# Performance work log

Hardware: AMD Instinct MI355X
Metric: run time of the kernel (lower is better)

## Reference

```python
import jax, jax.numpy as jnp
import numpy as np

NUM_HEADS = 16
ROPE_BASE = 10000.0


def _rope_cos_sin(seq_len, head_dim, dtype):
    inv_freq = 1.0 / (ROPE_BASE ** (jnp.arange(0, head_dim, 2, dtype=jnp.float32) / head_dim))
    freqs = jnp.arange(seq_len, dtype=jnp.float32)[:, None] * inv_freq[None, :]  # [L, hd/2]
    return jnp.cos(freqs).astype(dtype), jnp.sin(freqs).astype(dtype)


def _apply_rope(t, cos, sin):
    # t: [B, H, L, hd]; cos/sin: [L, hd/2] broadcast over B,H
    x1 = t[..., ::2]
    x2 = t[..., 1::2]
    r1 = x1 * cos - x2 * sin
    r2 = x1 * sin + x2 * cos
    return jnp.stack([r1, r2], axis=-1).reshape(t.shape)


def setup_inputs() -> dict:
    key = jax.random.key(0)
    k1, k2, k3 = jax.random.split(key, 3)
    B, L, D = 2, 2048, 1024
    x = jax.random.normal(k1, (B, L, D), dtype=jnp.float32)
    W_qkv = jax.random.normal(k2, (3 * D, D), dtype=jnp.float32) * (D ** -0.5)
    W_out = jax.random.normal(k3, (D, D), dtype=jnp.float32) * (D ** -0.5)
    return {"x": x, "W_qkv": W_qkv, "W_out": W_out}


def reference(x, W_qkv, W_out):
    B, L, D = x.shape
    H = NUM_HEADS
    hd = D // H
    scale = hd ** -0.5

    qkv = x @ W_qkv.T                              # [B, L, 3D]
    qkv = qkv.reshape(B, L, 3, H, hd)
    qkv = jnp.transpose(qkv, (2, 0, 3, 1, 4))      # [3, B, H, L, hd]
    q, k, v = qkv[0], qkv[1], qkv[2]

    cos, sin = _rope_cos_sin(L, hd, x.dtype)
    q = _apply_rope(q, cos, sin)
    k = _apply_rope(k, cos, sin)

    logits = jnp.einsum("bhqd,bhkd->bhqk", q, k) * scale
    attn = jax.nn.softmax(logits, axis=-1)         # dropout p=0.0 -> identity
    out = jnp.einsum("bhqk,bhkd->bhqd", attn, v)   # [B, H, L, hd]
    out = jnp.transpose(out, (0, 2, 1, 3)).reshape(B, L, D)
    return out @ W_out.T
```

## Files before the change

### kernel.cpp

```cpp
#include <hip/hip_runtime.h>
#include <hip/hip_bf16.h>
#include <stdint.h>


typedef __bf16 bf16x8 __attribute__((ext_vector_type(8)));
typedef float f32x4 __attribute__((ext_vector_type(4)));

__device__ __forceinline__ unsigned short f2bf(float f) {
  union { float f; unsigned int u; } v; v.f = f;
  unsigned int r = v.u + 0x7FFFu + ((v.u >> 16) & 1u);
  return (unsigned short)(r >> 16);
}
__device__ __forceinline__ float b2f(unsigned short u) {
  union { unsigned int u; float f; } v; v.u = ((unsigned int)u) << 16;
  return v.f;
}

__device__ __forceinline__ void gl2lds16(const void* gptr, void* lptr) {
  __builtin_amdgcn_global_load_lds(
      (const __attribute__((address_space(1))) unsigned int*)gptr,
      (__attribute__((address_space(3))) unsigned int*)lptr, 16, 0, 0);
}

__global__ void cvt_all(const float4* __restrict__ x,
                        const float4* __restrict__ wq,
                        const float4* __restrict__ wo,
                        ushort4* __restrict__ xb,
                        ushort4* __restrict__ wqb,
                        ushort4* __restrict__ wob) {
  int i = blockIdx.x * 256 + threadIdx.x;
  float4 v; ushort4* dst; int j;
  if (i < 1048576)      { v = x[i];            dst = xb;  j = i; }
  else if (i < 1835008) { v = wq[i - 1048576]; dst = wqb; j = i - 1048576; }
  else                  { v = wo[i - 1835008]; dst = wob; j = i - 1835008; }
  ushort4 o;
  o.x = f2bf(v.x); o.y = f2bf(v.y); o.z = f2bf(v.z); o.w = f2bf(v.w);
  dst[j] = o;
}

__global__ __launch_bounds__(256) void gemm_bt(
    const __hip_bfloat16* __restrict__ A,
    const __hip_bfloat16* __restrict__ B,
    unsigned short* __restrict__ C, int M, int N, int K) {
  __shared__ __align__(16) char lds[32768];
  const int tid = threadIdx.x;
  const int lane = tid & 63;
  const int wave = tid >> 6;
  const int wm = (wave >> 1) * 64, wn = (wave & 1) * 64;
  const int g = lane >> 4, lr = lane & 15;
  const int m0 = blockIdx.y * 128, n0 = blockIdx.x * 128;
  f32x4 acc[4][4] = {};

  const size_t ldb = (size_t)K * 2;
  const int c0 = tid, c1 = tid + 256;
  const int r0 = c0 >> 2, cb0 = (c0 & 3) * 16;
  const int r1 = c1 >> 2, cb1 = (c1 & 3) * 16;
  const char* A0 = (const char*)(A + (size_t)m0 * K) + (size_t)r0 * ldb + cb0;
  const char* A1 = (const char*)(A + (size_t)m0 * K) + (size_t)r1 * ldb + cb1;
  const char* B0 = (const char*)(B + (size_t)n0 * K) + (size_t)r0 * ldb + cb0;
  const char* B1 = (const char*)(B + (size_t)n0 * K) + (size_t)r1 * ldb + cb1;

  auto stage = [&](int bo) {
    gl2lds16(A0, lds + bo + c0 * 16);
    gl2lds16(A1, lds + bo + c1 * 16);
    gl2lds16(B0, lds + bo + 8192 + c0 * 16);
    gl2lds16(B1, lds + bo + 8192 + c1 * 16);
    A0 += 64; A1 += 64; B0 += 64; B1 += 64;
  };

  stage(0);

  const int NSTEP = K / 32;
  for (int kt = 0; kt < NSTEP; ++kt) {
    const int bo = (kt & 1) * 16384;
    if (kt + 1 < NSTEP) {
      stage(bo ^ 16384);
      asm volatile("s_waitcnt vmcnt(4)" ::: "memory");
    } else {
      asm volatile("s_waitcnt vmcnt(0)" ::: "memory");
    }
    __builtin_amdgcn_s_barrier();

    bf16x8 af[4], bfr[4];
#pragma unroll
    for (int i = 0; i < 4; ++i)
      af[i] = *(const bf16x8*)(lds + bo + (wm + i * 16 + lr) * 64 + g * 16);
#pragma unroll
    for (int i = 0; i < 4; ++i)
      bfr[i] = *(const bf16x8*)(lds + bo + 8192 + (wn + i * 16 + lr) * 64 + g * 16);
    __builtin_amdgcn_s_setprio(1);
#pragma unroll
    for (int i = 0; i < 4; ++i)
#pragma unroll
      for (int j = 0; j < 4; ++j)
        acc[i][j] = __builtin_amdgcn_mfma_f32_16x16x32_bf16(af[i], bfr[j], acc[i][j], 0, 0, 0);
    __builtin_amdgcn_s_setprio(0);
    asm volatile("s_waitcnt lgkmcnt(0)" ::: "memory");
    __builtin_amdgcn_s_barrier();
  }

#pragma unroll
  for (int i = 0; i < 4; ++i) {
#pragma unroll
    for (int j = 0; j < 4; ++j) {
      int n = n0 + wn + j * 16 + lr;
#pragma unroll
      for (int r = 0; r < 4; ++r) {
        int m = m0 + wm + i * 16 + g * 4 + r;
        C[(size_t)m * N + n] = f2bf(acc[i][j][r]);
      }
    }
  }
}

__global__ __launch_bounds__(256) void gemm2_64(
    const __hip_bfloat16* __restrict__ A,
    const __hip_bfloat16* __restrict__ B,
    float* __restrict__ C, int M, int N, int K) {
  __shared__ __align__(16) char lds[16384];
  const int tid = threadIdx.x, lane = tid & 63, w = tid >> 6;
  const int g = lane >> 4, lr = lane & 15;
  const int n0 = blockIdx.x * 64, m0 = blockIdx.y * 64;
  f32x4 acc[4] = {};

  const size_t ld = (size_t)K * 2;
  const int o16 = tid * 16;
  const int s = o16 ^ (((o16 >> 6) & 3) << 4);
  const int srow = s >> 6, scolb = s & 63;
  const char* Asrc = (const char*)(A + (size_t)m0 * K) + (size_t)srow * ld + scolb;
  const char* Bsrc = (const char*)(B + (size_t)n0 * K) + (size_t)srow * ld + scolb;

  auto stage = [&](int bo) {
    gl2lds16(Asrc, lds + bo + o16);
    gl2lds16(Bsrc, lds + 8192 + bo + o16);
    Asrc += 64; Bsrc += 64;
  };

  stage(0);

  const int swz = (lr & 3) << 4;
  const int NSTEP = K / 32;
  for (int kt = 0; kt < NSTEP; ++kt) {
    const int bo = (kt & 1) * 4096;
    if (kt + 1 < NSTEP) {
      stage(bo ^ 4096);
      asm volatile("s_waitcnt vmcnt(2)" ::: "memory");
    } else {
      asm volatile("s_waitcnt vmcnt(0)" ::: "memory");
    }
    __builtin_amdgcn_s_barrier();

    bf16x8 af = *(const bf16x8*)(lds + bo + (((w * 16 + lr) * 64 + g * 16) ^ swz));
    __builtin_amdgcn_s_setprio(1);
#pragma unroll
    for (int j = 0; j < 4; ++j) {
      bf16x8 bf = *(const bf16x8*)(lds + 8192 + bo + (((j * 16 + lr) * 64 + g * 16) ^ swz));
      acc[j] = __builtin_amdgcn_mfma_f32_16x16x32_bf16(af, bf, acc[j], 0, 0, 0);
    }
    __builtin_amdgcn_s_setprio(0);
    asm volatile("s_waitcnt lgkmcnt(0)" ::: "memory");
    __builtin_amdgcn_s_barrier();
  }

#pragma unroll
  for (int j = 0; j < 4; ++j) {
    int n = n0 + j * 16 + lr;
#pragma unroll
    for (int r = 0; r < 4; ++r) {
      int m = m0 + w * 16 + g * 4 + r;
      C[(size_t)m * N + n] = acc[j][r];
    }
  }
}

__global__ void rope_scatter(const __hip_bfloat16* __restrict__ qkv,
                             __hip_bfloat16* __restrict__ Qs,
                             __hip_bfloat16* __restrict__ Ks,
                             __hip_bfloat16* __restrict__ Vt) {
  const int t = blockIdx.x * 256 + threadIdx.x;
  const int i = t & 31;
  const int lc = (t >> 5) & 255;
  const int h = (t >> 13) & 15;
  const int b = t >> 17;
  const float inv_freq = powf(10000.0f, -(float)i * (1.0f / 32.0f));
  const float QSCALE = 0.125f * 1.44269504088896f;
  const unsigned short* qk = (const unsigned short*)qkv;
  unsigned short v0[8], v1[8];
#pragma unroll
  for (int j = 0; j < 8; ++j) {
    const int l = lc * 8 + j;
    const size_t row = ((size_t)(b * 2048 + l)) * 3072;
    float s, c;
    sincosf((float)l * inv_freq, &s, &c);
    ushort2 qp = *(const ushort2*)(qk + row + h * 64 + 2 * i);
    ushort2 kp = *(const ushort2*)(qk + row + 1024 + h * 64 + 2 * i);
    ushort2 vp = *(const ushort2*)(qk + row + 2048 + h * 64 + 2 * i);
    float x1 = b2f(qp.x), x2 = b2f(qp.y);
    float y1 = b2f(kp.x), y2 = b2f(kp.y);
    size_t oidx = (((size_t)(b * 16 + h)) * 2048 + l) * 64 + 2 * i;
    ushort2 qo, ko;
    qo.x = f2bf((x1 * c - x2 * s) * QSCALE);
    qo.y = f2bf((x1 * s + x2 * c) * QSCALE);
    ko.x = f2bf(y1 * c - y2 * s);
    ko.y = f2bf(y1 * s + y2 * c);
    *(ushort2*)((unsigned short*)Qs + oidx) = qo;
    *(ushort2*)((unsigned short*)Ks + oidx) = ko;
    v0[j] = vp.x; v1[j] = vp.y;
  }
  const int m = lc & 3;
  const int colA = ((m & 1) << 4) + ((m >> 1) << 2);
  unsigned short* Vtu = (unsigned short*)Vt;
  const size_t vrow0 = (((size_t)(b * 16 + h)) * 64 + 2 * i) * 2048 + (lc >> 2) * 32;
  const size_t vrow1 = vrow0 + 2048;
  *(ushort4*)(Vtu + vrow0 + colA)     = make_ushort4(v0[0], v0[1], v0[2], v0[3]);
  *(ushort4*)(Vtu + vrow0 + colA + 8) = make_ushort4(v0[4], v0[5], v0[6], v0[7]);
  *(ushort4*)(Vtu + vrow1 + colA)     = make_ushort4(v1[0], v1[1], v1[2], v1[3]);
  *(ushort4*)(Vtu + vrow1 + colA + 8) = make_ushort4(v1[4], v1[5], v1[6], v1[7]);
}

__global__ __launch_bounds__(256, 4) void attn_fwd(
    const __hip_bfloat16* __restrict__ Qs,
    const __hip_bfloat16* __restrict__ Ks,
    const __hip_bfloat16* __restrict__ Vt,
    float* __restrict__ Opart,
    float2* __restrict__ Ml) {
  constexpr int L = 2048;
  __shared__ __align__(16) char lds[32768];
  const int tid = threadIdx.x, lane = tid & 63, w = tid >> 6;
  const int g = lane >> 4, lr = lane & 15;
  const int blk = blockIdx.x;
  const int xcd = blk & 7, slot = blk >> 3;
  const int bh = xcd * 4 + (slot >> 5);
  const int rem = slot & 31;
  const int qt = rem >> 1, half = rem & 1;
  const int q0 = qt * 128 + w * 32 + lr;
  const int kt0 = half * 16;

  const __hip_bfloat16* Qr = Qs + ((size_t)bh * L + q0) * 64;
  bf16x8 qf[2][2];
  qf[0][0] = *(const bf16x8*)(Qr + g * 8);
  qf[0][1] = *(const bf16x8*)(Qr + 32 + g * 8);
  qf[1][0] = *(const bf16x8*)(Qr + 16 * 64 + g * 8);
  qf[1][1] = *(const bf16x8*)(Qr + 16 * 64 + 32 + g * 8);

  bf16x8 onesf;
#pragma unroll
  for (int j = 0; j < 8; ++j) onesf[j] = (__bf16)1.0f;

  const int xmask = (lr & 7) << 4;
  const int loff0 = ((g * 16) ^ (xmask & 0x30)) + (xmask & 0x40);
  const int kb0 = lr * 128 + loff0;
  const int kb1 = kb0 ^ 64;

  const int c0 = tid * 16, c1 = c0 + 4096;
  const int os0 = c0 ^ (((c0 >> 7) & 7) << 4);
  const int os1 = c1 ^ (((c1 >> 7) & 7) << 4);
  const char* Kb = (const char*)(Ks + (size_t)bh * L * 64) + (size_t)kt0 * 8192;
  const char* Vb = (const char*)(Vt + (size_t)bh * 64 * L) + kt0 * 128;
  const char* KsrcA = Kb + os0;
  const char* KsrcB = Kb + os1;
  const char* VsrcA = Vb + (size_t)(os0 >> 7) * (L * 2) + (os0 & 127);
  const char* VsrcB = Vb + (size_t)(os1 >> 7) * (L * 2) + (os1 & 127);

  auto stage = [&](int bo) {
    gl2lds16(KsrcA, lds + bo + c0);
    gl2lds16(KsrcB, lds + bo + c1);
    gl2lds16(VsrcA, lds + 16384 + bo + c0);
    gl2lds16(VsrcB, lds + 16384 + bo + c1);
    KsrcA += 8192; KsrcB += 8192; VsrcA += 128; VsrcB += 128;
  };

  f32x4 oacc[2][4] = {};
  f32x4 lacc[2] = {};
  float mrun[2] = {-1e30f, -1e30f};

  stage(0);

  for (int kt = 0; kt < 16; ++kt) {
    const int bo = (kt & 1) * 8192;
    if (kt + 1 < 16) {
      stage(bo ^ 8192);
      asm volatile("s_waitcnt vmcnt(4)" ::: "memory");
    } else {
      asm volatile("s_waitcnt vmcnt(0)" ::: "memory");
    }
    __builtin_amdgcn_s_barrier();

    const char* Kc = lds + bo;
    const char* Vc = lds + 16384 + bo;

    f32x4 sacc[2][4] = {};
    __builtin_amdgcn_s_setprio(1);
#pragma unroll
    for (int mf = 0; mf < 4; ++mf) {
      bf16x8 a0 = *(const bf16x8*)(Kc + kb0 + mf * 2048);
      bf16x8 a1 = *(const bf16x8*)(Kc + kb1 + mf * 2048);
      sacc[0][mf] = __builtin_amdgcn_mfma_f32_16x16x32_bf16(a0, qf[0][0], sacc[0][mf], 0, 0, 0);
      sacc[0][mf] = __builtin_amdgcn_mfma_f32_16x16x32_bf16(a1, qf[0][1], sacc[0][mf], 0, 0, 0);
      sacc[1][mf] = __builtin_amdgcn_mfma_f32_16x16x32_bf16(a0, qf[1][0], sacc[1][mf], 0, 0, 0);
      sacc[1][mf] = __builtin_amdgcn_mfma_f32_16x16x32_bf16(a1, qf[1][1], sacc[1][mf], 0, 0, 0);
    }
    __builtin_amdgcn_s_setprio(0);

#pragma unroll
    for (int qg = 0; qg < 2; ++qg) {
      float a0 = fmaxf(fmaxf(sacc[qg][0][0], sacc[qg][0][1]), sacc[qg][0][2]);
      float a1 = fmaxf(fmaxf(sacc[qg][0][3], sacc[qg][1][0]), sacc[qg][1][1]);
      float a2 = fmaxf(fmaxf(sacc[qg][1][2], sacc[qg][1][3]), sacc[qg][2][0]);
      float a3 = fmaxf(fmaxf(sacc[qg][2][1], sacc[qg][2][2]), sacc[qg][2][3]);
      float a4 = fmaxf(fmaxf(sacc[qg][3][0], sacc[qg][3][1]), sacc[qg][3][2]);
      float b0 = fmaxf(fmaxf(a0, a1), a2);
      float b1 = fmaxf(fmaxf(a3, a4), sacc[qg][3][3]);
      float lmax = fmaxf(b0, b1);
      if (__any(lmax > mrun[qg] + 8.0f)) {
        float tmax = fmaxf(lmax, __shfl_xor(lmax, 16));
        tmax = fmaxf(tmax, __shfl_xor(tmax, 32));
        float mnew = fmaxf(mrun[qg], tmax);
        float al = __builtin_amdgcn_exp2f(mrun[qg] - mnew);
        mrun[qg] = mnew;
        lacc[qg] *= al;
#pragma unroll
        for (int d = 0; d < 4; ++d) oacc[qg][d] = oacc[qg][d] * al;
      }
#pragma unroll
      for (int mf = 0; mf < 4; ++mf) {
        sacc[qg][mf][0] = __builtin_amdgcn_exp2f(sacc[qg][mf][0] - mrun[qg]);
        sacc[qg][mf][1] = __builtin_amdgcn_exp2f(sacc[qg][mf][1] - mrun[qg]);
        sacc[qg][mf][2] = __builtin_amdgcn_exp2f(sacc[qg][mf][2] - mrun[qg]);
        sacc[qg][mf][3] = __builtin_amdgcn_exp2f(sacc[qg][mf][3] - mrun[qg]);
      }
    }

#pragma unroll
    for (int ks = 0; ks < 2; ++ks) {
      bf16x8 pf[2];
#pragma unroll
      for (int qg = 0; qg < 2; ++qg) {
#pragma unroll
        for (int j = 0; j < 4; ++j) {
          pf[qg][j]     = (__bf16)sacc[qg][2 * ks][j];
          pf[qg][4 + j] = (__bf16)sacc[qg][2 * ks + 1][j];
        }
      }
      const int kb = ks ? kb1 : kb0;
      __builtin_amdgcn_s_setprio(1);
      lacc[0] = __builtin_amdgcn_mfma_f32_16x16x32_bf16(onesf, pf[0], lacc[0], 0, 0, 0);
      lacc[1] = __builtin_amdgcn_mfma_f32_16x16x32_bf16(onesf, pf[1], lacc[1], 0, 0, 0);
#pragma unroll
      for (int df = 0; df < 4; ++df) {
        bf16x8 a = *(const bf16x8*)(Vc + kb + df * 2048);
        oacc[0][df] = __builtin_amdgcn_mfma_f32_16x16x32_bf16(a, pf[0], oacc[0][df], 0, 0, 0);
        oacc[1][df] = __builtin_amdgcn_mfma_f32_16x16x32_bf16(a, pf[1], oacc[1][df], 0, 0, 0);
      }
      __builtin_amdgcn_s_setprio(0);
    }
    asm volatile("s_waitcnt lgkmcnt(0)" ::: "memory");
    __builtin_amdgcn_s_barrier();
  }

#pragma unroll
  for (int qg = 0; qg < 2; ++qg) {
    const size_t rowi = ((size_t)bh * L + q0 + qg * 16) * 2 + half;
    float* Od = Opart + rowi * 64;
#pragma unroll
    for (int df = 0; df < 4; ++df)
      *(f32x4*)(Od + df * 16 + g * 4) = oacc[qg][df];
    if (g == 0) {
      float2 ml; ml.x = mrun[qg]; ml.y = lacc[qg][0];
      Ml[rowi] = ml;
    }
  }
}

__global__ __launch_bounds__(256) void attn_reduce(
    const float* __restrict__ Opart, const float2* __restrict__ Ml,
    unsigned short* __restrict__ Ob) {
  int t = blockIdx.x * 256 + threadIdx.x;
  int d = t & 63;
  int r = t >> 6;
  float2 a = Ml[2 * r], b = Ml[2 * r + 1];
  float m = fmaxf(a.x, b.x);
  float w0 = __builtin_amdgcn_exp2f(a.x - m);
  float w1 = __builtin_amdgcn_exp2f(b.x - m);
  float l = a.y * w0 + b.y * w1;
  float o = Opart[(size_t)(2 * r) * 64 + d] * w0 + Opart[(size_t)(2 * r + 1) * 64 + d] * w1;
  float out = o / l;
  int bh = r >> 11, qq = r & 2047;
  Ob[(((size_t)(bh >> 4) * 2048 + qq)) * 1024 + (bh & 15) * 64 + d] = f2bf(out);
}

extern "C" void kernel_launch(void* const* d_in, const int* in_sizes, int n_in,
                              void* d_out, int out_size, void* d_ws, size_t ws_size,
                              hipStream_t stream) {
  (void)in_sizes; (void)n_in; (void)out_size; (void)ws_size;
  const float* x    = (const float*)d_in[0];
  const float* wqkv = (const float*)d_in[1];
  const float* wout = (const float*)d_in[2];

  char* ws = (char*)d_ws;
  auto* wob   = (__hip_bfloat16*)(ws + ((size_t)0u  << 20));
  auto* Qsb   = (__hip_bfloat16*)(ws + ((size_t)2u  << 20));
  auto* Ob    = (__hip_bfloat16*)(ws + ((size_t)2u  << 20));
  auto* Ksb   = (__hip_bfloat16*)(ws + ((size_t)10u << 20));
  auto* Vtb   = (__hip_bfloat16*)(ws + ((size_t)18u << 20));
  auto* qkvb  = (__hip_bfloat16*)(ws + ((size_t)26u << 20));
  auto* Opart = (float*)         (ws + ((size_t)26u << 20));
  auto* xb    = (__hip_bfloat16*)(ws + ((size_t)50u << 20));
  auto* wqb   = (__hip_bfloat16*)(ws + ((size_t)58u << 20));
  auto* Mlp   = (float2*)        (ws + ((size_t)58u << 20));

  cvt_all<<<8192, 256, 0, stream>>>((const float4*)x, (const float4*)wqkv,
                                    (const float4*)wout,
                                    (ushort4*)xb, (ushort4*)wqb, (ushort4*)wob);
  gemm_bt<<<dim3(24, 32), 256, 0, stream>>>(xb, wqb, (unsigned short*)qkvb,
                                            4096, 3072, 1024);
  rope_scatter<<<1024, 256, 0, stream>>>(qkvb, Qsb, Ksb, Vtb);
  attn_fwd<<<1024, 256, 0, stream>>>(Qsb, Ksb, Vtb, Opart, Mlp);
  attn_reduce<<<16384, 256, 0, stream>>>(Opart, Mlp, (unsigned short*)Ob);
  gemm2_64<<<dim3(16, 64), 256, 0, stream>>>(Ob, wob, (float*)d_out,
                                             4096, 1024, 1024);
}
```

Before: 133.5 us.

## Fuse RoPE, Q/K scatter and V transpose into QKV GEMM epilogue

Result: no change. 131.0 us (-1.8%).

```diff
diff --git a/kernel.cpp b/kernel.cpp
--- a/kernel.cpp
+++ b/kernel.cpp
@@ -27,8 +27,18 @@
                         const float4* __restrict__ wo,
                         ushort4* __restrict__ xb,
                         ushort4* __restrict__ wqb,
-                        ushort4* __restrict__ wob) {
+                        ushort4* __restrict__ wob,
+                        float2* __restrict__ tab) {
   int i = blockIdx.x * 256 + threadIdx.x;
+  if (i >= 2097152) {
+    int t = i - 2097152;
+    int l = t >> 5, fi = t & 31;
+    float inv_freq = powf(10000.0f, -(float)fi / 32.0f);
+    float s, c;
+    sincosf((float)l * inv_freq, &s, &c);
+    tab[t] = make_float2(c, s);
+    return;
+  }
   float4 v; ushort4* dst; int j;
   if (i < 1048576)      { v = x[i];            dst = xb;  j = i; }
   else if (i < 1835008) { v = wq[i - 1048576]; dst = wqb; j = i - 1048576; }
@@ -38,10 +48,13 @@
   dst[j] = o;
 }
 
-__global__ __launch_bounds__(256) void gemm_bt(
+__global__ __launch_bounds__(256) void gemm1_fused(
     const __hip_bfloat16* __restrict__ A,
     const __hip_bfloat16* __restrict__ B,
-    unsigned short* __restrict__ C, int M, int N, int K) {
+    unsigned short* __restrict__ Qs,
+    unsigned short* __restrict__ Ks,
+    unsigned short* __restrict__ Vt,
+    const float2* __restrict__ tab, int K) {
   __shared__ __align__(16) char lds[32768];
   const int tid = threadIdx.x;
   const int lane = tid & 63;
@@ -99,15 +112,44 @@
     __builtin_amdgcn_s_barrier();
   }
 
-#pragma unroll
-  for (int i = 0; i < 4; ++i) {
+  const int sel = n0 >> 10;
+  if (sel <= 1) {
+    const float qscale = (sel == 0) ? 0.125f * 1.44269504088896f : 1.0f;
+    unsigned short* dst = (sel == 0) ? Qs : Ks;
 #pragma unroll
     for (int j = 0; j < 4; ++j) {
-      int n = n0 + wn + j * 16 + lr;
-#pragma unroll
-      for (int r = 0; r < 4; ++r) {
-        int m = m0 + wm + i * 16 + g * 4 + r;
-        C[(size_t)m * N + n] = f2bf(acc[i][j][r]);
+      const int nn = (n0 + wn + j * 16 + lr) & 1023;
+      const int h = nn >> 6, d = nn & 63;
+      const float2* tabrow = tab + (d >> 1);
+      const float sgn = (d & 1) ? 1.0f : -1.0f;
+#pragma unroll
+      for (int i = 0; i < 4; ++i) {
+#pragma unroll
+        for (int r = 0; r < 4; ++r) {
+          const int m = m0 + wm + i * 16 + g * 4 + r;
+          const int l = m & 2047, b = m >> 11;
+          float own = acc[i][j][r];
+          float part = __shfl_xor(own, 1);
+          float2 cs = tabrow[l * 32];
+          float out = fmaf(cs.x, own, sgn * cs.y * part) * qscale;
+          dst[((size_t)((b * 16 + h) * 2048 + l)) * 64 + d] = f2bf(out);
+        }
+      }
+    }
+  } else {
+#pragma unroll
+    for (int j = 0; j < 4; ++j) {
+      const int nn = (n0 + wn + j * 16 + lr) & 1023;
+      const int h = nn >> 6, d = nn & 63;
+#pragma unroll
+      for (int i = 0; i < 4; ++i) {
+        const int mb = m0 + wm + i * 16 + g * 4;
+        const int l0 = mb & 2047, b = mb >> 11;
+        const int pl = (l0 & ~31) + 8 * ((l0 & 15) >> 2) + 4 * ((l0 >> 4) & 1) + (l0 & 3);
+        ushort4 v4;
+        v4.x = f2bf(acc[i][j][0]); v4.y = f2bf(acc[i][j][1]);
+        v4.z = f2bf(acc[i][j][2]); v4.w = f2bf(acc[i][j][3]);
+        *(ushort4*)(Vt + ((size_t)((b * 16 + h) * 64 + d)) * 2048 + pl) = v4;
       }
     }
   }
@@ -171,51 +213,6 @@
       C[(size_t)m * N + n] = acc[j][r];
     }
   }
-}
-
-__global__ void rope_scatter(const __hip_bfloat16* __restrict__ qkv,
-                             __hip_bfloat16* __restrict__ Qs,
-                             __hip_bfloat16* __restrict__ Ks,
-                             __hip_bfloat16* __restrict__ Vt) {
-  const int t = blockIdx.x * 256 + threadIdx.x;
-  const int i = t & 31;
-  const int lc = (t >> 5) & 255;
-  const int h = (t >> 13) & 15;
-  const int b = t >> 17;
-  const float inv_freq = powf(10000.0f, -(float)i * (1.0f / 32.0f));
-  const float QSCALE = 0.125f * 1.44269504088896f;
-  const unsigned short* qk = (const unsigned short*)qkv;
-  unsigned short v0[8], v1[8];
-#pragma unroll
-  for (int j = 0; j < 8; ++j) {
-    const int l = lc * 8 + j;
-    const size_t row = ((size_t)(b * 2048 + l)) * 3072;
-    float s, c;
-    sincosf((float)l * inv_freq, &s, &c);
-    ushort2 qp = *(const ushort2*)(qk + row + h * 64 + 2 * i);
-    ushort2 kp = *(const ushort2*)(qk + row + 1024 + h * 64 + 2 * i);
-    ushort2 vp = *(const ushort2*)(qk + row + 2048 + h * 64 + 2 * i);
-    float x1 = b2f(qp.x), x2 = b2f(qp.y);
-    float y1 = b2f(kp.x), y2 = b2f(kp.y);
-    size_t oidx = (((size_t)(b * 16 + h)) * 2048 + l) * 64 + 2 * i;
-    ushort2 qo, ko;
-    qo.x = f2bf((x1 * c - x2 * s) * QSCALE);
-    qo.y = f2bf((x1 * s + x2 * c) * QSCALE);
-    ko.x = f2bf(y1 * c - y2 * s);
-    ko.y = f2bf(y1 * s + y2 * c);
-    *(ushort2*)((unsigned short*)Qs + oidx) = qo;
-    *(ushort2*)((unsigned short*)Ks + oidx) = ko;
-    v0[j] = vp.x; v1[j] = vp.y;
-  }
-  const int m = lc & 3;
-  const int colA = ((m & 1) << 4) + ((m >> 1) << 2);
-  unsigned short* Vtu = (unsigned short*)Vt;
-  const size_t vrow0 = (((size_t)(b * 16 + h)) * 64 + 2 * i) * 2048 + (lc >> 2) * 32;
-  const size_t vrow1 = vrow0 + 2048;
-  *(ushort4*)(Vtu + vrow0 + colA)     = make_ushort4(v0[0], v0[1], v0[2], v0[3]);
-  *(ushort4*)(Vtu + vrow0 + colA + 8) = make_ushort4(v0[4], v0[5], v0[6], v0[7]);
-  *(ushort4*)(Vtu + vrow1 + colA)     = make_ushort4(v1[0], v1[1], v1[2], v1[3]);
-  *(ushort4*)(Vtu + vrow1 + colA + 8) = make_ushort4(v1[4], v1[5], v1[6], v1[7]);
 }
 
 __global__ __launch_bounds__(256, 4) void attn_fwd(
@@ -403,18 +400,21 @@
   auto* Ob    = (__hip_bfloat16*)(ws + ((size_t)2u  << 20));
   auto* Ksb   = (__hip_bfloat16*)(ws + ((size_t)10u << 20));
   auto* Vtb   = (__hip_bfloat16*)(ws + ((size_t)18u << 20));
-  auto* qkvb  = (__hip_bfloat16*)(ws + ((size_t)26u << 20));
   auto* Opart = (float*)         (ws + ((size_t)26u << 20));
   auto* xb    = (__hip_bfloat16*)(ws + ((size_t)50u << 20));
-  auto* wqb   = (__hip_bfloat16*)(ws + ((size_t)58u << 20));
   auto* Mlp   = (float2*)        (ws + ((size_t)58u << 20));
-
-  cvt_all<<<8192, 256, 0, stream>>>((const float4*)x, (const float4*)wqkv,
+  auto* tab   = (float2*)        (ws + ((size_t)59u << 20));
+  auto* wqb   = (__hip_bfloat16*)(ws + (((size_t)59u << 20) + ((size_t)1u << 19)));
+
+  cvt_all<<<8448, 256, 0, stream>>>((const float4*)x, (const float4*)wqkv,
                                     (const float4*)wout,
-                                    (ushort4*)xb, (ushort4*)wqb, (ushort4*)wob);
-  gemm_bt<<<dim3(24, 32), 256, 0, stream>>>(xb, wqb, (unsigned short*)qkvb,
-                                            4096, 3072, 1024);
-  rope_scatter<<<1024, 256, 0, stream>>>(qkvb, Qsb, Ksb, Vtb);
+                                    (ushort4*)xb, (ushort4*)wqb, (ushort4*)wob,
+                                    tab);
+  gemm1_fused<<<dim3(24, 32), 256, 0, stream>>>(xb, wqb,
+                                                (unsigned short*)Qsb,
+                                                (unsigned short*)Ksb,
+                                                (unsigned short*)Vtb,
+                                                tab, 1024);
   attn_fwd<<<1024, 256, 0, stream>>>(Qsb, Ksb, Vtb, Opart, Mlp);
   attn_reduce<<<16384, 256, 0, stream>>>(Opart, Mlp, (unsigned short*)Ob);
   gemm2_64<<<dim3(16, 64), 256, 0, stream>>>(Ob, wob, (float*)d_out,
```
